# Performance work log

Measured on AMD Instinct MI355X. Metric: run time of the kernel, lower is better.

Reference implementation:

```python
import jax, jax.numpy as jnp
import numpy as np

NB_HEADS = 12


def setup_inputs() -> dict:
    key = jax.random.key(0)
    ks = jax.random.split(key, 6)
    B, S, D, H = 4, 1024, 768, NB_HEADS
    x = jax.random.normal(ks[0], (B, S, D), dtype=jnp.float32)
    Wqkv = jax.random.normal(ks[1], (D, 3 * D), dtype=jnp.float32) * 0.02
    bqkv = jnp.zeros((3 * D,), dtype=jnp.float32)
    Wl = jax.random.normal(ks[2], (H, H), dtype=jnp.float32) * 0.3
    bl = jnp.zeros((H,), dtype=jnp.float32)
    Ww = jax.random.normal(ks[3], (H, H), dtype=jnp.float32) * 0.3
    bw = jnp.zeros((H,), dtype=jnp.float32)
    Wproj = jax.random.normal(ks[4], (D, D), dtype=jnp.float32) * 0.02
    bproj = jnp.zeros((D,), dtype=jnp.float32)
    return {"x": x, "Wqkv": Wqkv, "bqkv": bqkv, "Wl": Wl, "bl": bl,
            "Ww": Ww, "bw": bw, "Wproj": Wproj, "bproj": bproj}


def reference(x, Wqkv, bqkv, Wl, bl, Ww, bw, Wproj, bproj):
    B, S, D = x.shape
    H = NB_HEADS
    dh = D // H
    scale = dh ** (-0.5)
    # qkv projection: [B,S,3D] -> [3,B,H,S,dh]
    qkv = (x @ Wqkv + bqkv).reshape(B, S, 3, H, dh).transpose(2, 0, 3, 1, 4)
    q, k, v = qkv[0] * scale, qkv[1], qkv[2]
    # raw attention logits [B,H,S,S]
    attn = jnp.einsum('bhqd,bhkd->bhqk', q, k)
    # pre-softmax talking-heads mix across head dim (Dense over heads)
    attn = jnp.einsum('bhqk,hg->bgqk', attn, Wl) + bl[None, :, None, None]
    attn = jax.nn.softmax(attn, axis=-1)
    # post-softmax talking-heads mix
    attn = jnp.einsum('bhqk,hg->bgqk', attn, Ww) + bw[None, :, None, None]
    # attention-weighted values -> [B,S,D]
    out = jnp.einsum('bhqk,bhkd->bqhd', attn, v).reshape(B, S, D)
    return out @ Wproj + bproj
```

## Files before the change

### kernel.cpp

```cpp
#include <hip/hip_runtime.h>
#include <cstdint>

#define BB 4
#define SS 1024
#define DD 768
#define HH 12
#define DH 64

typedef unsigned short u16;
typedef unsigned int   u32;
typedef __attribute__((ext_vector_type(8))) short bf16x8;
typedef __attribute__((ext_vector_type(4))) float f32x4;

__device__ __forceinline__ u16 f2bf(float f) {
    u32 u = __float_as_uint(f);
    u += 0x7fffu + ((u >> 16) & 1u);
    return (u16)(u >> 16);
}
__device__ __forceinline__ float b2f(u32 lo16) {
    return __uint_as_float(lo16 << 16);
}

__device__ __forceinline__ float fast_exp2(float x) {
    return __builtin_amdgcn_exp2f(x);
}

#if __has_builtin(__builtin_amdgcn_cvt_pk_bf16_f32)
__device__ __forceinline__ u32 pack2(float a, float b) {
    auto r = __builtin_amdgcn_cvt_pk_bf16_f32(a, b);
    u32 v; __builtin_memcpy(&v, &r, 4); return v;
}
#else
__device__ __forceinline__ u32 pack2(float a, float b) {
    return (u32)f2bf(a) | ((u32)f2bf(b) << 16);
}
#endif

#define ASYNC16(gp, lp) __builtin_amdgcn_global_load_lds( \
    (const __attribute__((address_space(1))) void*)(gp),  \
    (__attribute__((address_space(3))) void*)(lp), 16, 0, 0)

template<int BM_, int BN_, class Epi>
__device__ __forceinline__ void mfma_gemm(
    const u16* __restrict__ A, const u16* __restrict__ B,
    int K, int lda, int ldb, int m0, int n0, const Epi& epi)
{
    constexpr int MI = BM_ / 32;
    constexpr int NJ = BN_ / 32;
    __shared__ u16 Alds[BM_ * 32];
    __shared__ u16 Blds[BN_ * 32];

    const int tid  = threadIdx.x;
    const int wave = tid >> 6;
    const int lane = tid & 63;
    const int wr = wave >> 1, wc = wave & 1;

    const int ar = lane >> 2;
    const int ac = (lane & 3) * 8;

    f32x4 acc[MI][NJ] = {};

    for (int k0 = 0; k0 < K; k0 += 32) {
        __syncthreads();
#pragma unroll
        for (int j = 0; j < BM_ / 64; ++j) {
            const int rb = wave * (BM_ / 4) + j * 16;
            ASYNC16(A + (size_t)(m0 + rb + ar) * lda + k0 + ac, &Alds[rb * 32]);
        }
#pragma unroll
        for (int j = 0; j < BN_ / 64; ++j) {
            const int rb = wave * (BN_ / 4) + j * 16;
            ASYNC16(B + (size_t)(n0 + rb + ar) * ldb + k0 + ac, &Blds[rb * 32]);
        }
        __syncthreads();

        bf16x8 af[MI], bfr[NJ];
#pragma unroll
        for (int mi = 0; mi < MI; ++mi)
            af[mi] = *(const bf16x8*)&Alds[(wr * (BM_ / 2) + mi * 16 + (lane & 15)) * 32 + (lane >> 4) * 8];
#pragma unroll
        for (int nj = 0; nj < NJ; ++nj)
            bfr[nj] = *(const bf16x8*)&Blds[(wc * (BN_ / 2) + nj * 16 + (lane & 15)) * 32 + (lane >> 4) * 8];
#pragma unroll
        for (int mi = 0; mi < MI; ++mi)
#pragma unroll
            for (int nj = 0; nj < NJ; ++nj)
                acc[mi][nj] = __builtin_amdgcn_mfma_f32_16x16x32_bf16(
                    af[mi], bfr[nj], acc[mi][nj], 0, 0, 0);
    }

#pragma unroll
    for (int mi = 0; mi < MI; ++mi)
#pragma unroll
        for (int nj = 0; nj < NJ; ++nj)
#pragma unroll
            for (int r = 0; r < 4; ++r)
                epi(m0 + wr * (BM_ / 2) + mi * 16 + (lane >> 4) * 4 + r,
                    n0 + wc * (BN_ / 2) + nj * 16 + (lane & 15),
                    acc[mi][nj][r]);
}

#define CPAD 136

__global__ __launch_bounds__(256) void qkv_gemm_kernel(
    const u16* __restrict__ xb, const u16* __restrict__ Wt,
    const float* __restrict__ bias,
    u16* __restrict__ qb, u16* __restrict__ kb, u16* __restrict__ vb)
{
    __shared__ u16 Alds[128 * 32];
    __shared__ u16 Blds[128 * 32];
    __shared__ u16 Clds[128 * CPAD];

    const int tid  = threadIdx.x;
    const int wave = tid >> 6;
    const int lane = tid & 63;
    const int wr = wave >> 1, wc = wave & 1;
    const int ar = lane >> 2;
    const int ac = (lane & 3) * 8;
    const int m0 = blockIdx.y * 128, n0 = blockIdx.x * 128;

    f32x4 acc[4][4] = {};

    for (int k0 = 0; k0 < DD; k0 += 32) {
        __syncthreads();
#pragma unroll
        for (int j = 0; j < 2; ++j) {
            const int rb = wave * 32 + j * 16;
            ASYNC16(xb + (size_t)(m0 + rb + ar) * DD + k0 + ac, &Alds[rb * 32]);
            ASYNC16(Wt + (size_t)(n0 + rb + ar) * DD + k0 + ac, &Blds[rb * 32]);
        }
        __syncthreads();

        bf16x8 af[4], bfr[4];
#pragma unroll
        for (int mi = 0; mi < 4; ++mi)
            af[mi] = *(const bf16x8*)&Alds[(wr * 64 + mi * 16 + (lane & 15)) * 32 + (lane >> 4) * 8];
#pragma unroll
        for (int nj = 0; nj < 4; ++nj)
            bfr[nj] = *(const bf16x8*)&Blds[(wc * 64 + nj * 16 + (lane & 15)) * 32 + (lane >> 4) * 8];
#pragma unroll
        for (int mi = 0; mi < 4; ++mi)
#pragma unroll
            for (int nj = 0; nj < 4; ++nj)
                acc[mi][nj] = __builtin_amdgcn_mfma_f32_16x16x32_bf16(
                    af[mi], bfr[nj], acc[mi][nj], 0, 0, 0);
    }

    const int c  = n0 / DD;
    const int w0 = n0 - c * DD;
    const int hA = w0 >> 6;
    const float qs = (c == 0) ? 0.125f : 1.0f;
#pragma unroll
    for (int mi = 0; mi < 4; ++mi)
#pragma unroll
        for (int nj = 0; nj < 4; ++nj)
#pragma unroll
            for (int r = 0; r < 4; ++r) {
                const int row = wr * 64 + mi * 16 + (lane >> 4) * 4 + r;
                const int col = wc * 64 + nj * 16 + (lane & 15);
                Clds[row * CPAD + col] = f2bf((acc[mi][nj][r] + bias[n0 + col]) * qs);
            }
    __syncthreads();

    u16* const dst = (c == 0) ? qb : (c == 1) ? kb : vb;
    const int b = m0 >> 10;
#pragma unroll
    for (int j = 0; j < 8; ++j) {
        const int idx = j * 256 + tid;
        const int row = idx >> 4, u4 = idx & 15;
        const int half = u4 >> 3, d8 = u4 & 7;
        const int h = hA + half;
        const int s = (m0 + row) & 1023;
        const uint4 v = *(const uint4*)&Clds[row * CPAD + half * 64 + d8 * 8];
        *(uint4*)&dst[(((size_t)(b * HH + h) << 10) + s) * DH + d8 * 8] = v;
    }
}

__global__ __launch_bounds__(256) void vtrans_kernel(
    const u16* __restrict__ vb, u16* __restrict__ vt)
{
    __shared__ u16 t[64 * 72];
    const int tid = threadIdx.x;
    const int bh = blockIdx.y;
    const int s0 = blockIdx.x * 64;
    const u16* src = vb + ((size_t)bh << 16) + (size_t)s0 * DH;

#pragma unroll
    for (int j = 0; j < 2; ++j) {
        const int idx = j * 256 + tid;
        const int row = idx >> 3, u4 = idx & 7;
        *(uint4*)&t[row * 72 + u4 * 8] = *(const uint4*)&src[row * DH + u4 * 8];
    }
    __syncthreads();

#pragma unroll
    for (int j = 0; j < 2; ++j) {
        const int idx = j * 256 + tid;
        const int d = idx >> 3, u4 = idx & 7;
        u16 tmp[8];
#pragma unroll
        for (int i = 0; i < 8; ++i) tmp[i] = t[(u4 * 8 + i) * 72 + d];
        *(uint4*)&vt[((size_t)bh * DH + d) * SS + s0 + u4 * 8] = *(const uint4*)tmp;
    }
}

__global__ __launch_bounds__(256) void qk_gemm_kernel(
    const u16* __restrict__ qb, const u16* __restrict__ kb,
    u16* __restrict__ attn, int bh0)
{
    __shared__ u16 Alds[128 * 32];
    __shared__ u16 Blds[128 * 32];
    __shared__ u16 Clds[128 * CPAD];

    const int tid  = threadIdx.x;
    const int wave = tid >> 6;
    const int lane = tid & 63;
    const int wr = wave >> 1, wc = wave & 1;
    const int ar = lane >> 2;
    const int ac = (lane & 3) * 8;
    const int m0 = blockIdx.y * 128, n0 = blockIdx.x * 128;

    const int bhL = blockIdx.z;
    const u16* A = qb + (size_t)(bh0 + bhL) * SS * DH;
    const u16* B = kb + (size_t)(bh0 + bhL) * SS * DH;
    u16* C = attn + (size_t)bhL * SS * SS;

    f32x4 acc[4][4] = {};

#pragma unroll
    for (int k0 = 0; k0 < DH; k0 += 32) {
        __syncthreads();
#pragma unroll
        for (int j = 0; j < 2; ++j) {
            const int rb = wave * 32 + j * 16;
            ASYNC16(A + (size_t)(m0 + rb + ar) * DH + k0 + ac, &Alds[rb * 32]);
            ASYNC16(B + (size_t)(n0 + rb + ar) * DH + k0 + ac, &Blds[rb * 32]);
        }
        __syncthreads();

        bf16x8 af[4], bfr[4];
#pragma unroll
        for (int mi = 0; mi < 4; ++mi)
            af[mi] = *(const bf16x8*)&Alds[(wr * 64 + mi * 16 + (lane & 15)) * 32 + (lane >> 4) * 8];
#pragma unroll
        for (int nj = 0; nj < 4; ++nj)
            bfr[nj] = *(const bf16x8*)&Blds[(wc * 64 + nj * 16 + (lane & 15)) * 32 + (lane >> 4) * 8];
#pragma unroll
        for (int mi = 0; mi < 4; ++mi)
#pragma unroll
            for (int nj = 0; nj < 4; ++nj)
                acc[mi][nj] = __builtin_amdgcn_mfma_f32_16x16x32_bf16(
                    af[mi], bfr[nj], acc[mi][nj], 0, 0, 0);
    }

#pragma unroll
    for (int mi = 0; mi < 4; ++mi)
#pragma unroll
        for (int nj = 0; nj < 4; ++nj)
#pragma unroll
            for (int r = 0; r < 4; ++r) {
                const int row = wr * 64 + mi * 16 + (lane >> 4) * 4 + r;
                const int col = wc * 64 + nj * 16 + (lane & 15);
                Clds[row * CPAD + col] = f2bf(acc[mi][nj][r]);
            }
    __syncthreads();

#pragma unroll
    for (int j = 0; j < 8; ++j) {
        const int idx = j * 256 + tid;
        const int row = idx >> 4, u4 = idx & 15;
        *(uint4*)&C[(size_t)(m0 + row) * SS + n0 + u4 * 8] =
            *(const uint4*)&Clds[row * CPAD + u4 * 8];
    }
}

__global__ __launch_bounds__(256) void pv_gemm_kernel(
    const u16* __restrict__ attn2, const u16* __restrict__ vt,
    u16* __restrict__ ctx, int bh0)
{
    const int bhL = blockIdx.z;
    const int bh = bh0 + bhL;
    const int b = bh / HH, h = bh % HH;
    const u16* A = attn2 + (size_t)bhL * SS * SS;
    const u16* B = vt + (size_t)bh * DH * SS;
    u16* C = ctx + (size_t)b * SS * DD + h * DH;
    struct Epi {
        u16* C;
        __device__ void operator()(int m, int n, float v) const {
            C[(size_t)m * DD + n] = f2bf(v);
        }
    } epi{C};
    mfma_gemm<64, 64>(A, B, SS, SS, SS, blockIdx.y * 64, 0, epi);
}

__global__ __launch_bounds__(256) void proj_gemm_kernel(
    const u16* __restrict__ ctx, const u16* __restrict__ Wt,
    const float* __restrict__ bias, float* __restrict__ out)
{
    struct Epi {
        float* out; const float* bias;
        __device__ void operator()(int m, int n, float v) const {
            out[(size_t)m * DD + n] = v + bias[n];
        }
    } epi{out, bias};
    mfma_gemm<128, 64>(ctx, Wt, DD, DD, DD, blockIdx.y * 128, blockIdx.x * 64, epi);
}

#define BLKU 4104

__device__ __forceinline__ int physIdx(int r, int half) {
    return (r & 3) * BLKU + (r >> 2) * 16 + ((half ^ ((r >> 2) & 1)) << 3);
}

__global__ __launch_bounds__(256) void mix_softmax_kernel(
    const u16* __restrict__ attn, u16* __restrict__ attn2,
    const float* __restrict__ Wl, const float* __restrict__ bl,
    const float* __restrict__ Ww, const float* __restrict__ bw)
{
    __shared__ u16 buf[4 * BLKU];
    __shared__ float wsum[4][16];
    __shared__ float invd[16];

    const int tid  = threadIdx.x;
    const int wave = tid >> 6;
    const int lane = tid & 63;
    const int u    = lane >> 4;
    const int ln   = lane & 15;
    const int bL = blockIdx.x >> 10;
    const int qi = blockIdx.x & (SS - 1);
    const size_t gbase = ((size_t)bL * HH * SS + qi) * SS + tid * 4;

    {
        uint2 src[HH];
#pragma unroll
        for (int h = 0; h < HH; ++h)
            src[h] = *(const uint2*)&attn[gbase + (size_t)h * SS * SS];

#pragma unroll
        for (int i = 0; i < 4; ++i) {
            const u32 sel = (i & 1) ? 0x07060302u : 0x05040100u;
            u32 w[6];
#pragma unroll
            for (int j = 0; j < 6; ++j) {
                const u32 lo = (i < 2) ? src[2 * j].x     : src[2 * j].y;
                const u32 hi = (i < 2) ? src[2 * j + 1].x : src[2 * j + 1].y;
                w[j] = __builtin_amdgcn_perm(hi, lo, sel);
            }
            uint4 q0; q0.x = w[0]; q0.y = w[1]; q0.z = w[2]; q0.w = w[3];
            uint4 q1; q1.x = w[4]; q1.y = w[5]; q1.z = 0u;   q1.w = 0u;
            const int r = 4 * tid + i;
            *(uint4*)&buf[physIdx(r, 0)] = q0;
            *(uint4*)&buf[physIdx(r, 1)] = q1;
        }
    }

    bf16x8 a1;
    {
        u16 t[8];
#pragma unroll
        for (int j = 0; j < 8; ++j) {
            const int k = u * 8 + j;
            t[j] = (k < HH && ln < HH) ? f2bf(Wl[k * HH + ln] * 1.44269504f) : (u16)0;
        }
        __builtin_memcpy(&a1, t, 16);
    }
    f32x4 c1 = {0.f, 0.f, 0.f, 0.f};
#pragma unroll
    for (int r = 0; r < 4; ++r) {
        const int g = u * 4 + r;
        c1[r] = (g < HH) ? bl[g] * 1.44269504f : 0.f;
    }

    __syncthreads();

    const int posbase = wave * 256;
    const int uh = u & 1;

    float part[4] = {0.f, 0.f, 0.f, 0.f};
#pragma unroll
    for (int mi = 0; mi < 16; ++mi) {
        const int r = posbase + mi * 16 + ln;
        const bf16x8 bfrag = *(const bf16x8*)&buf[physIdx(r, uh)];
        const f32x4 d = __builtin_amdgcn_mfma_f32_16x16x32_bf16(a1, bfrag, c1, 0, 0, 0);
        const float e0 = fast_exp2(d[0]);
        const float e1 = fast_exp2(d[1]);
        const float e2 = fast_exp2(d[2]);
        const float e3 = fast_exp2(d[3]);
        part[0] += e0; part[1] += e1; part[2] += e2; part[3] += e3;
        if (u < 3) {
            uint2 p;
            p.x = pack2(e0, e1); p.y = pack2(e2, e3);
            *(uint2*)&buf[physIdx(r, u >> 1) + (u & 1) * 4] = p;
        }
    }

#pragma unroll
    for (int off = 1; off < 16; off <<= 1) {
#pragma unroll
        for (int r = 0; r < 4; ++r) part[r] += __shfl_xor(part[r], off);
    }
    if (ln == 0) {
#pragma unroll
        for (int r = 0; r < 4; ++r) wsum[wave][u * 4 + r] = part[r];
    }
    __syncthreads();
    if (tid < 16)
        invd[tid] = 1.0f / (wsum[0][tid] + wsum[1][tid] + wsum[2][tid] + wsum[3][tid]);
    __syncthreads();

    bf16x8 a2;
    {
        u16 t[8];
#pragma unroll
        for (int j = 0; j < 8; ++j) {
            const int k = u * 8 + j;
            t[j] = (k < HH && ln < HH) ? f2bf(Ww[k * HH + ln] * invd[k]) : (u16)0;
        }
        __builtin_memcpy(&a2, t, 16);
    }
    f32x4 c2 = {0.f, 0.f, 0.f, 0.f};
#pragma unroll
    for (int r = 0; r < 4; ++r) {
        const int g = u * 4 + r;
        c2[r] = (g < HH) ? bw[g] : 0.f;
    }

#pragma unroll
    for (int mi = 0; mi < 16; ++mi) {
        const int r = posbase + mi * 16 + ln;
        const bf16x8 bfrag = *(const bf16x8*)&buf[physIdx(r, uh)];
        const f32x4 d = __builtin_amdgcn_mfma_f32_16x16x32_bf16(a2, bfrag, c2, 0, 0, 0);
        if (u < 3) {
            uint2 p;
            p.x = pack2(d[0], d[1]); p.y = pack2(d[2], d[3]);
            *(uint2*)&buf[physIdx(r, u >> 1) + (u & 1) * 4] = p;
        }
    }
    __syncthreads();

    {
        u32 rw[4][6];
#pragma unroll
        for (int i = 0; i < 4; ++i) {
            const int r = 4 * tid + i;
            const uint4 a = *(const uint4*)&buf[physIdx(r, 0)];
            const uint2 b = *(const uint2*)&buf[physIdx(r, 1)];
            rw[i][0] = a.x; rw[i][1] = a.y; rw[i][2] = a.z;
            rw[i][3] = a.w; rw[i][4] = b.x; rw[i][5] = b.y;
        }
#pragma unroll
        for (int g = 0; g < HH; ++g) {
            const u32 sel = (g & 1) ? 0x07060302u : 0x05040100u;
            uint2 p;
            p.x = __builtin_amdgcn_perm(rw[1][g >> 1], rw[0][g >> 1], sel);
            p.y = __builtin_amdgcn_perm(rw[3][g >> 1], rw[2][g >> 1], sel);
            *(uint2*)&attn2[gbase + (size_t)g * SS * SS] = p;
        }
    }
}


__global__ __launch_bounds__(256) void cvt_bf16_kernel(
    const float* __restrict__ in, u16* __restrict__ out, int n8)
{
    const int i = blockIdx.x * 256 + threadIdx.x;
    if (i >= n8) return;
    const float4 a = ((const float4*)in)[i * 2];
    const float4 b = ((const float4*)in)[i * 2 + 1];
    uint4 p;
    p.x = pack2(a.x, a.y); p.y = pack2(a.z, a.w);
    p.z = pack2(b.x, b.y); p.w = pack2(b.z, b.w);
    ((uint4*)out)[i] = p;
}

__global__ __launch_bounds__(256) void cvt_transpose_kernel(
    const float* __restrict__ in, u16* __restrict__ out, int R, int C)
{
    __shared__ float t[32][33];
    const int c0 = blockIdx.x * 32, r0 = blockIdx.y * 32;
    const int tr = threadIdx.x >> 3;
    const int tc = (threadIdx.x & 7) * 4;
    const float4 v = *(const float4*)&in[(size_t)(r0 + tr) * C + c0 + tc];
    t[tc + 0][tr] = v.x; t[tc + 1][tr] = v.y;
    t[tc + 2][tr] = v.z; t[tc + 3][tr] = v.w;
    __syncthreads();
    uint2 p;
    p.x = pack2(t[tr][tc + 0], t[tr][tc + 1]);
    p.y = pack2(t[tr][tc + 2], t[tr][tc + 3]);
    *(uint2*)&out[(size_t)(c0 + tr) * R + r0 + tc] = p;
}

extern "C" void kernel_launch(void* const* d_in, const int* in_sizes, int n_in,
                              void* d_out, int out_size, void* d_ws, size_t ws_size,
                              hipStream_t stream)
{
    const float* x     = (const float*)d_in[0];
    const float* Wqkv  = (const float*)d_in[1];
    const float* bqkv  = (const float*)d_in[2];
    const float* Wl    = (const float*)d_in[3];
    const float* bl    = (const float*)d_in[4];
    const float* Ww    = (const float*)d_in[5];
    const float* bw    = (const float*)d_in[6];
    const float* Wproj = (const float*)d_in[7];
    const float* bproj = (const float*)d_in[8];
    float* out = (float*)d_out;

    const size_t N_XB  = (size_t)BB * SS * DD;
    const size_t N_QB  = (size_t)BB * HH * SS * DH;
    const size_t N_WT  = (size_t)DD * 3 * DD;
    const size_t N_WP  = (size_t)DD * DD;
    const size_t N_AT1 = (size_t)HH * SS * SS;

    u16* xb  = (u16*)d_ws;
    u16* qb  = xb  + N_XB;
    u16* kb  = qb  + N_QB;
    u16* vb  = kb  + N_QB;
    u16* vt  = vb  + N_QB;
    u16* ctx = vt  + N_QB;
    u16* Wqkv_t = ctx + N_XB;
    u16* Wproj_t = Wqkv_t + N_WT;
    u16* attn = Wproj_t + N_WP;

    const size_t fixed_bytes = (size_t)(N_XB * 2 + N_QB * 4 + N_WT + N_WP) * 2;
    int b_per = BB;
    while (b_per > 1 &&
           fixed_bytes + (size_t)b_per * N_AT1 * 2 * 2 > ws_size)
        b_per >>= 1;
    const int n_iter = BB / b_per;
    u16* attn2 = attn + (size_t)b_per * N_AT1;

    const dim3 blk(256);

    cvt_bf16_kernel<<<dim3((N_XB / 8 + 255) / 256), blk, 0, stream>>>(x, xb, (int)(N_XB / 8));
    cvt_transpose_kernel<<<dim3(3 * DD / 32, DD / 32), blk, 0, stream>>>(Wqkv, Wqkv_t, DD, 3 * DD);
    cvt_transpose_kernel<<<dim3(DD / 32, DD / 32), blk, 0, stream>>>(Wproj, Wproj_t, DD, DD);

    qkv_gemm_kernel<<<dim3(3 * DD / 128, BB * SS / 128), blk, 0, stream>>>(
        xb, Wqkv_t, bqkv, qb, kb, vb);
    vtrans_kernel<<<dim3(SS / 64, BB * HH), blk, 0, stream>>>(vb, vt);

    for (int it = 0; it < n_iter; ++it) {
        const int bh0 = it * b_per * HH;
        qk_gemm_kernel<<<dim3(SS / 128, SS / 128, b_per * HH), blk, 0, stream>>>(
            qb, kb, attn, bh0);
        mix_softmax_kernel<<<dim3(b_per * SS), blk, 0, stream>>>(
            attn, attn2, Wl, bl, Ww, bw);
        pv_gemm_kernel<<<dim3(1, SS / 64, b_per * HH), blk, 0, stream>>>(
            attn2, vt, ctx, bh0);
    }

    proj_gemm_kernel<<<dim3(DD / 64, BB * SS / 128), blk, 0, stream>>>(
        ctx, Wproj_t, bproj, out);
}
```

Baseline: 240.9 us.

## Use 32x32 MFMA in mix-softmax, keep exps in registers, write attn in place

The head-mixing softmax kernel switches from 16x16x32 to 32x32x16 bf16 MFMA tiles. The exponentiated values stay in registers and are exchanged with lane shuffles, replacing the LDS write-back between the two mixes, and a barrier is dropped. The LDS row stride padding also changes, and the mixed output now overwrites the attention buffer in place, which halves workspace and may allow more batches per iteration. The risks are wasted MFMA work on the padded 12-of-32 rows, and correctness that relies on each wave reading only LDS rows it wrote itself.

```diff
diff --git a/kernel.cpp b/kernel.cpp
--- a/kernel.cpp
+++ b/kernel.cpp
@@ -11,6 +11,7 @@
 typedef unsigned int   u32;
 typedef __attribute__((ext_vector_type(8))) short bf16x8;
 typedef __attribute__((ext_vector_type(4))) float f32x4;
+typedef __attribute__((ext_vector_type(16))) float f32x16;
 
 __device__ __forceinline__ u16 f2bf(float f) {
     u32 u = __float_as_uint(f);
@@ -306,7 +307,7 @@
     mfma_gemm<128, 64>(ctx, Wt, DD, DD, DD, blockIdx.y * 128, blockIdx.x * 64, epi);
 }
 
-#define BLKU 4104
+#define BLKU 4112
 
 __device__ __forceinline__ int physIdx(int r, int half) {
     return (r & 3) * BLKU + (r >> 2) * 16 + ((half ^ ((r >> 2) & 1)) << 3);
@@ -324,8 +325,8 @@
     const int tid  = threadIdx.x;
     const int wave = tid >> 6;
     const int lane = tid & 63;
-    const int u    = lane >> 4;
-    const int ln   = lane & 15;
+    const int l31  = lane & 31;
+    const int hi   = lane >> 5;
     const int bL = blockIdx.x >> 10;
     const int qi = blockIdx.x & (SS - 1);
     const size_t gbase = ((size_t)bL * HH * SS + qi) * SS + tid * 4;
@@ -343,8 +344,8 @@
 #pragma unroll
             for (int j = 0; j < 6; ++j) {
                 const u32 lo = (i < 2) ? src[2 * j].x     : src[2 * j].y;
-                const u32 hi = (i < 2) ? src[2 * j + 1].x : src[2 * j + 1].y;
-                w[j] = __builtin_amdgcn_perm(hi, lo, sel);
+                const u32 hh = (i < 2) ? src[2 * j + 1].x : src[2 * j + 1].y;
+                w[j] = __builtin_amdgcn_perm(hh, lo, sel);
             }
             uint4 q0; q0.x = w[0]; q0.y = w[1]; q0.z = w[2]; q0.w = w[3];
             uint4 q1; q1.x = w[4]; q1.y = w[5]; q1.z = 0u;   q1.w = 0u;
@@ -359,52 +360,55 @@
         u16 t[8];
 #pragma unroll
         for (int j = 0; j < 8; ++j) {
-            const int k = u * 8 + j;
-            t[j] = (k < HH && ln < HH) ? f2bf(Wl[k * HH + ln] * 1.44269504f) : (u16)0;
+            const int k = hi * 8 + j;
+            t[j] = (k < HH && l31 < HH) ? f2bf(Wl[k * HH + l31] * 1.44269504f) : (u16)0;
         }
         __builtin_memcpy(&a1, t, 16);
     }
-    f32x4 c1 = {0.f, 0.f, 0.f, 0.f};
-#pragma unroll
-    for (int r = 0; r < 4; ++r) {
-        const int g = u * 4 + r;
-        c1[r] = (g < HH) ? bl[g] * 1.44269504f : 0.f;
-    }
-
+    f32x16 c1;
+#pragma unroll
+    for (int r = 0; r < 16; ++r) {
+        const int row = (r & 3) + 8 * (r >> 2) + 4 * hi;
+        c1[r] = (row < HH) ? bl[row] * 1.44269504f : 0.f;
+    }
+
+    const int posbase = wave * 256;
+
+    u32 Rc[8][4];
+    float dacc[8] = {0.f, 0.f, 0.f, 0.f, 0.f, 0.f, 0.f, 0.f};
+#pragma unroll
+    for (int c = 0; c < 8; ++c) {
+        const int r = posbase + c * 32 + l31;
+        const bf16x8 bfrag = *(const bf16x8*)&buf[physIdx(r, hi)];
+        const f32x16 d = __builtin_amdgcn_mfma_f32_32x32x16_bf16(a1, bfrag, c1, 0, 0, 0);
+        float e[8];
+#pragma unroll
+        for (int j = 0; j < 8; ++j) e[j] = fast_exp2(d[j]);
+        dacc[0] += e[0]; dacc[1] += e[1]; dacc[2] += e[2]; dacc[3] += e[3];
+        if (lane < 32) {
+            dacc[4] += e[4]; dacc[5] += e[5]; dacc[6] += e[6]; dacc[7] += e[7];
+        }
+        Rc[c][0] = pack2(e[0], e[1]);
+        Rc[c][1] = pack2(e[2], e[3]);
+        Rc[c][2] = pack2(e[4], e[5]);
+        Rc[c][3] = pack2(e[6], e[7]);
+    }
+
+#pragma unroll
+    for (int off = 1; off < 32; off <<= 1) {
+#pragma unroll
+        for (int j = 0; j < 8; ++j) dacc[j] += __shfl_xor(dacc[j], off);
+    }
+    if (lane == 0) {
+#pragma unroll
+        for (int j = 0; j < 4; ++j) { wsum[wave][j] = dacc[j]; wsum[wave][8 + j] = dacc[4 + j]; }
+    }
+    if (lane == 32) {
+#pragma unroll
+        for (int j = 0; j < 4; ++j) wsum[wave][4 + j] = dacc[j];
+    }
     __syncthreads();
-
-    const int posbase = wave * 256;
-    const int uh = u & 1;
-
-    float part[4] = {0.f, 0.f, 0.f, 0.f};
-#pragma unroll
-    for (int mi = 0; mi < 16; ++mi) {
-        const int r = posbase + mi * 16 + ln;
-        const bf16x8 bfrag = *(const bf16x8*)&buf[physIdx(r, uh)];
-        const f32x4 d = __builtin_amdgcn_mfma_f32_16x16x32_bf16(a1, bfrag, c1, 0, 0, 0);
-        const float e0 = fast_exp2(d[0]);
-        const float e1 = fast_exp2(d[1]);
-        const float e2 = fast_exp2(d[2]);
-        const float e3 = fast_exp2(d[3]);
-        part[0] += e0; part[1] += e1; part[2] += e2; part[3] += e3;
-        if (u < 3) {
-            uint2 p;
-            p.x = pack2(e0, e1); p.y = pack2(e2, e3);
-            *(uint2*)&buf[physIdx(r, u >> 1) + (u & 1) * 4] = p;
-        }
-    }
-
-#pragma unroll
-    for (int off = 1; off < 16; off <<= 1) {
-#pragma unroll
-        for (int r = 0; r < 4; ++r) part[r] += __shfl_xor(part[r], off);
-    }
-    if (ln == 0) {
-#pragma unroll
-        for (int r = 0; r < 4; ++r) wsum[wave][u * 4 + r] = part[r];
-    }
-    __syncthreads();
-    if (tid < 16)
+    if (tid < HH)
         invd[tid] = 1.0f / (wsum[0][tid] + wsum[1][tid] + wsum[2][tid] + wsum[3][tid]);
     __syncthreads();
 
@@ -413,30 +417,43 @@
         u16 t[8];
 #pragma unroll
         for (int j = 0; j < 8; ++j) {
-            const int k = u * 8 + j;
-            t[j] = (k < HH && ln < HH) ? f2bf(Ww[k * HH + ln] * invd[k]) : (u16)0;
+            const int k = hi * 8 + j;
+            t[j] = (k < HH && l31 < HH) ? f2bf(Ww[k * HH + l31] * invd[k]) : (u16)0;
         }
         __builtin_memcpy(&a2, t, 16);
     }
-    f32x4 c2 = {0.f, 0.f, 0.f, 0.f};
-#pragma unroll
-    for (int r = 0; r < 4; ++r) {
-        const int g = u * 4 + r;
-        c2[r] = (g < HH) ? bw[g] : 0.f;
-    }
-
-#pragma unroll
-    for (int mi = 0; mi < 16; ++mi) {
-        const int r = posbase + mi * 16 + ln;
-        const bf16x8 bfrag = *(const bf16x8*)&buf[physIdx(r, uh)];
-        const f32x4 d = __builtin_amdgcn_mfma_f32_16x16x32_bf16(a2, bfrag, c2, 0, 0, 0);
-        if (u < 3) {
-            uint2 p;
-            p.x = pack2(d[0], d[1]); p.y = pack2(d[2], d[3]);
-            *(uint2*)&buf[physIdx(r, u >> 1) + (u & 1) * 4] = p;
-        }
-    }
-    __syncthreads();
+    f32x16 c2;
+#pragma unroll
+    for (int r = 0; r < 16; ++r) {
+        const int row = (r & 3) + 8 * (r >> 2) + 4 * hi;
+        c2[r] = (row < HH) ? bw[row] : 0.f;
+    }
+
+#pragma unroll
+    for (int c = 0; c < 8; ++c) {
+        const u32 w0 = Rc[c][0], w1 = Rc[c][1], w2 = Rc[c][2], w3 = Rc[c][3];
+        const u32 s0 = (u32)__shfl_xor((int)w0, 32);
+        const u32 s1 = (u32)__shfl_xor((int)w1, 32);
+        const u32 s2 = (u32)__shfl_xor((int)w2, 32);
+        const u32 s3 = (u32)__shfl_xor((int)w3, 32);
+        u32 bw_[4];
+        bw_[0] = hi ? s2 : w0;
+        bw_[1] = hi ? s3 : w1;
+        bw_[2] = s0;
+        bw_[3] = s1;
+        bf16x8 b2; __builtin_memcpy(&b2, bw_, 16);
+        const f32x16 d = __builtin_amdgcn_mfma_f32_32x32x16_bf16(a2, b2, c2, 0, 0, 0);
+
+        const int r = posbase + c * 32 + l31;
+        uint2 pA; pA.x = pack2(d[0], d[1]); pA.y = pack2(d[2], d[3]);
+        if (lane < 32) {
+            uint2 pB; pB.x = pack2(d[4], d[5]); pB.y = pack2(d[6], d[7]);
+            *(uint2*)&buf[physIdx(r, 0)] = pA;
+            *(uint2*)&buf[physIdx(r, 1)] = pB;
+        } else {
+            *(uint2*)&buf[physIdx(r, 0) + 4] = pA;
+        }
+    }
 
     {
         u32 rw[4][6];
@@ -524,10 +541,10 @@
     const size_t fixed_bytes = (size_t)(N_XB * 2 + N_QB * 4 + N_WT + N_WP) * 2;
     int b_per = BB;
     while (b_per > 1 &&
-           fixed_bytes + (size_t)b_per * N_AT1 * 2 * 2 > ws_size)
+           fixed_bytes + (size_t)b_per * N_AT1 * 2 > ws_size)
         b_per >>= 1;
     const int n_iter = BB / b_per;
-    u16* attn2 = attn + (size_t)b_per * N_AT1;
+    u16* attn2 = attn;
 
     const dim3 blk(256);
 
```

Result: no change. 244.7 us (+1.6%).
